# Optimization experiments

Measured on AMD Instinct MI355X. Metric: run time of the kernel, lower is better.

Reference implementation:

```python
import jax, jax.numpy as jnp
import numpy as np

D_MODEL = 2048
N_HEADS = 16
HEAD_DIM = D_MODEL // N_HEADS  # 128
SCALE_BASE = 512


def rotate_half(x):
    x1, x2 = jnp.split(x, 2, axis=-1)
    return jnp.concatenate((-x2, x1), axis=-1)


def rotary_xpos(seq_len, dim, dtype=jnp.float32):
    inv_freq = 1.0 / (10000.0 ** (jnp.arange(0, dim, 2, dtype=jnp.float32) / dim))
    t = jnp.arange(seq_len, dtype=jnp.float32)
    freqs = jnp.einsum('i,j->ij', t, inv_freq)
    freqs = jnp.concatenate((freqs, freqs), axis=-1)  # [S, dim]
    scale_base = (jnp.arange(0, dim, 2, dtype=jnp.float32) + 0.4 * dim) / (1.4 * dim)
    power = (t - seq_len // 2) / SCALE_BASE
    scale = scale_base[None, :] ** power[:, None]  # [S, dim/2]
    scale = jnp.concatenate((scale, scale), axis=-1)  # [S, dim]
    return freqs.astype(dtype), scale.astype(dtype)


def apply_rotary(t, pos, scale):
    return t * jnp.cos(pos) * scale + rotate_half(t) * jnp.sin(pos) * scale


def setup_inputs() -> dict:
    key = jax.random.key(0)
    ks = jax.random.split(key, 5)
    B, S = 2, 2048
    hidden_states = jax.random.normal(ks[0], (B, S, D_MODEL), dtype=jnp.float32)
    # Linear weights stored as [out, in] like torch; we use x @ W.T
    w_q = jax.random.normal(ks[1], (N_HEADS * HEAD_DIM, D_MODEL), dtype=jnp.float32) * 0.02
    w_kv = jax.random.normal(ks[2], (2 * HEAD_DIM, D_MODEL), dtype=jnp.float32) * 0.02
    w_proj = jax.random.normal(ks[3], (D_MODEL, N_HEADS * HEAD_DIM), dtype=jnp.float32) * 0.02
    b_proj = jax.random.normal(ks[4], (D_MODEL,), dtype=jnp.float32) * 0.02
    return {"hidden_states": hidden_states, "w_q": w_q, "w_kv": w_kv,
            "w_proj": w_proj, "b_proj": b_proj}


def reference(hidden_states, w_q, w_kv, w_proj, b_proj):
    B, S, _ = hidden_states.shape
    q = hidden_states @ w_q.T                      # [B,S,H*D]
    kv = hidden_states @ w_kv.T                    # [B,S,2*D]
    k, v = jnp.split(kv, 2, axis=-1)               # [B,S,D] each
    q = q.reshape(B, S, N_HEADS, HEAD_DIM).transpose(0, 2, 1, 3)  # [B,H,S,D]

    scale_w = HEAD_DIM ** (-0.5)
    q = q * scale_w
    k = k * scale_w

    pos, xscale = rotary_xpos(S, HEAD_DIM, q.dtype)
    q = apply_rotary(q, pos, xscale)               # broadcast [S,D] over [B,H,S,D]
    k = apply_rotary(k, pos, 1.0 / xscale)         # [B,S,D]

    attn = jnp.einsum('bnih,bjh->bnij', q, k)      # [B,H,S,S]
    causal = jnp.triu(jnp.ones((S, S), dtype=bool), 1)
    attn = jnp.where(causal, -jnp.finfo(attn.dtype).max, attn)
    attn = jax.nn.softmax(attn, axis=-1)

    out = jnp.einsum('bnij,bjd->bind', attn, v)    # [B,S,H,D]
    out = out.reshape(B, S, N_HEADS * HEAD_DIM)
    out = out @ w_proj.T + b_proj
    return out
```

## Files before the change

### kernel.cpp

```cpp
#include <hip/hip_runtime.h>
#include <math.h>

typedef __bf16 bf16;
typedef __bf16 bf16x8 __attribute__((ext_vector_type(8)));
typedef float f32x4 __attribute__((ext_vector_type(4)));

#define MFMA16(a, b, c) __builtin_amdgcn_mfma_f32_16x16x32_bf16((a), (b), (c), 0, 0, 0)

__device__ __forceinline__ float clampf(float v, float lo, float hi) {
  return fminf(fmaxf(v, lo), hi);
}

__device__ __forceinline__ void async_copy16(const void* g, void* l) {
  __builtin_amdgcn_global_load_lds(
      (__attribute__((address_space(1))) void*)g,
      (__attribute__((address_space(3))) void*)l,
      16, 0, 0);
}


__global__ void convert_bf16(const float* __restrict__ hs,
                             const float* __restrict__ wq,
                             const float* __restrict__ wkv,
                             const float* __restrict__ wproj,
                             bf16* __restrict__ hs_bf,
                             bf16* __restrict__ wqkv_bf,
                             bf16* __restrict__ wproj_bf) {
  const long long v = (long long)blockIdx.x * blockDim.x + threadIdx.x;
  const float* src;
  bf16* dst;
  long long off;
  if (v < 1048576) { src = hs; dst = hs_bf; off = v; }
  else if (v < 1572864) { src = wq; dst = wqkv_bf; off = v - 1048576; }
  else if (v < 1638400) { src = wkv; dst = wqkv_bf + 4194304; off = v - 1572864; }
  else { src = wproj; dst = wproj_bf; off = v - 1638400; }
  const f32x4* p = (const f32x4*)(src + off * 8);
  f32x4 f0 = p[0], f1 = p[1];
  bf16x8 r;
#pragma unroll
  for (int i = 0; i < 4; ++i) { r[i] = (bf16)f0[i]; r[i + 4] = (bf16)f1[i]; }
  *(bf16x8*)(dst + off * 8) = r;
}

__global__ __launch_bounds__(256, 2)
void gemm_qkv(const bf16* __restrict__ A, const bf16* __restrict__ Bw,
              bf16* __restrict__ Cq, bf16* __restrict__ Ckv) {
  const int K = 2048;
  __shared__ bf16 As[128 * 32];
  __shared__ bf16 Bs[128 * 32];
  const int tid = threadIdx.x;
  const int wave = tid >> 6, lane = tid & 63;
  const int quad = lane >> 4, l15 = lane & 15;
  const int r4 = lane >> 2, c4 = lane & 3;
  const int wm = wave >> 1, wn = wave & 1;
  const int orig = blockIdx.x + 18 * blockIdx.y;
  const int wgid = (orig & 7) * 72 + (orig >> 3);
  const int bx = wgid % 18;
  const int bm = (wgid / 18) * 128;
  const bf16* Bp = Bw + (size_t)bx * 128 * K;

  const f32x4 vzero = {0.f, 0.f, 0.f, 0.f};
  f32x4 acc[4][4];
#pragma unroll
  for (int i = 0; i < 4; ++i)
#pragma unroll
    for (int j = 0; j < 4; ++j) acc[i][j] = vzero;

  for (int kt = 0; kt < K; kt += 32) {
    __syncthreads();
#pragma unroll
    for (int q = 0; q < 2; ++q) {
      const int chunk = wave * 2 + q;
      const int row = chunk * 16 + r4;
      async_copy16(A + (size_t)(bm + row) * K + kt + c4 * 8, (char*)As + chunk * 1024);
      async_copy16(Bp + (size_t)row * K + kt + c4 * 8, (char*)Bs + chunk * 1024);
    }
    __syncthreads();
    bf16x8 af[4], bfr[4];
#pragma unroll
    for (int i = 0; i < 4; ++i)
      af[i] = *(const bf16x8*)((const char*)As + (wm * 64 + i * 16 + l15) * 64 + quad * 16);
#pragma unroll
    for (int i = 0; i < 4; ++i)
      bfr[i] = *(const bf16x8*)((const char*)Bs + (wn * 64 + i * 16 + l15) * 64 + quad * 16);
#pragma unroll
    for (int mi = 0; mi < 4; ++mi)
#pragma unroll
      for (int ni = 0; ni < 4; ++ni)
        acc[mi][ni] = MFMA16(af[mi], bfr[ni], acc[mi][ni]);
  }

  bf16* Cp;
  int ldc, cn;
  if (bx < 16) { Cp = Cq; ldc = 2048; cn = bx * 128; }
  else { Cp = Ckv; ldc = 256; cn = (bx - 16) * 128; }
#pragma unroll
  for (int mi = 0; mi < 4; ++mi)
#pragma unroll
    for (int ni = 0; ni < 4; ++ni) {
      const int col = cn + wn * 64 + ni * 16 + l15;
#pragma unroll
      for (int r = 0; r < 4; ++r) {
        const int row = bm + wm * 64 + mi * 16 + quad * 4 + r;
        Cp[(size_t)row * ldc + col] = (bf16)clampf(acc[mi][ni][r], -1000.f, 1000.f);
      }
    }
}

__global__ __launch_bounds__(256, 2)
void gemm_proj(const bf16* __restrict__ A, const bf16* __restrict__ Bw,
               const float* __restrict__ bias, float* __restrict__ C) {
  const int K = 2048;
  __shared__ bf16 As[128 * 32];
  __shared__ bf16 Bs[128 * 32];
  const int tid = threadIdx.x;
  const int wave = tid >> 6, lane = tid & 63;
  const int quad = lane >> 4, l15 = lane & 15;
  const int r4 = lane >> 2, c4 = lane & 3;
  const int wm = wave >> 1, wn = wave & 1;
  const int orig = blockIdx.x + 16 * blockIdx.y;
  const int wgid = (orig & 7) * 64 + (orig >> 3);
  const int bn = (wgid % 16) * 128;
  const int bm = (wgid / 16) * 128;
  const bf16* Bp = Bw + (size_t)bn * K;

  const f32x4 vzero = {0.f, 0.f, 0.f, 0.f};
  f32x4 acc[4][4];
#pragma unroll
  for (int i = 0; i < 4; ++i)
#pragma unroll
    for (int j = 0; j < 4; ++j) acc[i][j] = vzero;

  for (int kt = 0; kt < K; kt += 32) {
    __syncthreads();
#pragma unroll
    for (int q = 0; q < 2; ++q) {
      const int chunk = wave * 2 + q;
      const int row = chunk * 16 + r4;
      async_copy16(A + (size_t)(bm + row) * K + kt + c4 * 8, (char*)As + chunk * 1024);
      async_copy16(Bp + (size_t)row * K + kt + c4 * 8, (char*)Bs + chunk * 1024);
    }
    __syncthreads();
    bf16x8 af[4], bfr[4];
#pragma unroll
    for (int i = 0; i < 4; ++i)
      af[i] = *(const bf16x8*)((const char*)As + (wm * 64 + i * 16 + l15) * 64 + quad * 16);
#pragma unroll
    for (int i = 0; i < 4; ++i)
      bfr[i] = *(const bf16x8*)((const char*)Bs + (wn * 64 + i * 16 + l15) * 64 + quad * 16);
#pragma unroll
    for (int mi = 0; mi < 4; ++mi)
#pragma unroll
      for (int ni = 0; ni < 4; ++ni)
        acc[mi][ni] = MFMA16(af[mi], bfr[ni], acc[mi][ni]);
  }

#pragma unroll
  for (int mi = 0; mi < 4; ++mi)
#pragma unroll
    for (int ni = 0; ni < 4; ++ni) {
      const int col = bn + wn * 64 + ni * 16 + l15;
      const float bv = bias[col];
#pragma unroll
      for (int r = 0; r < 4; ++r) {
        const int row = bm + wm * 64 + mi * 16 + quad * 4 + r;
        C[(size_t)row * 2048 + col] = clampf(acc[mi][ni][r] + bv, -1000.f, 1000.f);
      }
    }
}

__global__ void rotary_kv(bf16* __restrict__ Ckv, bf16* __restrict__ VT) {
  const int row = blockIdx.x;
  const int b = row >> 11, s = row & 2047;
  const int t = threadIdx.x;

  if (t < 64) {
    const float power = (float)(s - 1024) * (1.0f / 512.0f);
    const float scale_w = 0.08838834764831845f;
    const float k_if = 0.2076205059304679f;
    const int j = t;
    const float pos = (float)s * exp2f(-k_if * (float)j);
    const float c = cosf(pos), sn = sinf(pos);
    const float sb = ((float)(2 * j) + 51.2f) * (1.0f / 179.2f);
    const float xs = exp2f(power * log2f(sb));
    const float f = scale_w / xs;
    const size_t kvb = (size_t)row * 256;
    const float k1 = (float)Ckv[kvb + j];
    const float k2 = (float)Ckv[kvb + j + 64];
    Ckv[kvb + j]      = (bf16)((k1 * c - k2 * sn) * f);
    Ckv[kvb + j + 64] = (bf16)((k2 * c + k1 * sn) * f);
  } else {
    const int d = (t - 64) * 2;
    const size_t kvb = (size_t)row * 256 + 128;
    VT[((size_t)b * 128 + d) * 2048 + s]     = Ckv[kvb + d];
    VT[((size_t)b * 128 + d + 1) * 2048 + s] = Ckv[kvb + d + 1];
  }
}

__global__ __launch_bounds__(512, 1)
void flash_attn(const bf16* __restrict__ Qp, const bf16* __restrict__ Kkv,
                const bf16* __restrict__ VT, bf16* __restrict__ O) {
  __shared__ bf16 Ks[2][4 * 64 * 32];
  __shared__ bf16 Vs[2][2 * 128 * 32];
  __shared__ bf16 Ps[8][1024];

  const int tid = threadIdx.x;
  const int wave = tid >> 6, lane = tid & 63;
  const int quad = lane >> 4, l15 = lane & 15;
  const int r4 = lane >> 2, c4 = lane & 3;
  const int bh = blockIdx.x, b = bh >> 4, h = bh & 15;
  const int y = blockIdx.y;
  const int nkvA = 2 * y + 2;
  const int wrow = wave * 16;

  const int ssw = (r4 >> 1) & 3;
  const int rsw = ((l15 >> 1) & 3) * 16;

  const bf16* Kb = Kkv + (size_t)b * 2048 * 256;
  const bf16* Vb = VT + (size_t)b * 128 * 2048;

  bf16x8 vones;
  {
    const bf16 ov = (bf16)((l15 == 0) ? 1.0f : 0.0f);
#pragma unroll
    for (int i = 0; i < 8; ++i) vones[i] = ov;
  }

  const f32x4 vzero = {0.f, 0.f, 0.f, 0.f};
  bf16x8 qa[4];
  f32x4 oacc[8];
  f32x4 lacc;

  auto load_q = [&](int q0) {
    const int s = q0 + wrow + l15;
#pragma unroll
    for (int ks = 0; ks < 4; ++ks)
      qa[ks] = *(const bf16x8*)(Qp + ((size_t)(b * 2048 + s)) * 2048 +
                                h * 128 + ks * 32 + quad * 8);
    const float power = (float)(s - 1024) * (1.0f / 512.0f);
    const float scale_w = 0.08838834764831845f;
    const float k_if = 0.2076205059304679f;
#pragma unroll
    for (int ks = 0; ks < 2; ++ks)
#pragma unroll
      for (int u = 0; u < 8; ++u) {
        const int j = ks * 32 + quad * 8 + u;
        const float pos = (float)s * exp2f(-k_if * (float)j);
        const float c = __cosf(pos), sn = __sinf(pos);
        const float sb = ((float)(2 * j) + 51.2f) * (1.0f / 179.2f);
        const float xs = exp2f(power * __log2f(sb));
        const float f = xs * scale_w;
        const float q1 = (float)qa[ks][u], q2 = (float)qa[ks + 2][u];
        qa[ks][u]     = (bf16)((q1 * c - q2 * sn) * f);
        qa[ks + 2][u] = (bf16)((q2 * c + q1 * sn) * f);
      }
  };
  auto reset_acc = [&]() {
    lacc = vzero;
#pragma unroll
    for (int n8 = 0; n8 < 8; ++n8) oacc[n8] = vzero;
  };

  auto stage = [&](int kv0, int buf) {
#pragma unroll
    for (int t = 0; t < 2; ++t) {
      const int ii = wave * 2 + t;
      const int p = ii >> 2, ch = ii & 3;
      async_copy16(Kb + (size_t)(kv0 + ch * 16 + r4) * 256 + p * 32 + (c4 ^ ssw) * 8,
                   (char*)Ks[buf] + ii * 1024);
    }
#pragma unroll
    for (int t = 0; t < 2; ++t) {
      const int ii = wave * 2 + t;
      const int pc = ii >> 3, ch = ii & 7;
      async_copy16(Vb + (size_t)(ch * 16 + r4) * 2048 + kv0 + pc * 32 + (c4 ^ ssw) * 8,
                   (char*)Vs[buf] + ii * 1024);
    }
  };

  auto epilogue = [&](int q0) {
#pragma unroll
    for (int r = 0; r < 4; ++r) {
      const float l = __shfl(lacc[r], lane & 48);
      const float inv = 1.0f / l;
      const int s = q0 + wrow + quad * 4 + r;
#pragma unroll
      for (int n8 = 0; n8 < 8; ++n8) {
        const int d = n8 * 16 + l15;
        O[((size_t)(b * 2048 + s)) * 2048 + h * 128 + d] = (bf16)(oacc[n8][r] * inv);
      }
    }
  };

  int q0 = y * 128;
  load_q(q0);
  reset_acc();
  stage(0, 0);

  for (int jt = 0; jt < 34; ++jt) {
    const int kv0 = (jt < nkvA ? jt : jt - nkvA) * 64;
    const int buf = jt & 1;
    __syncthreads();
    if (jt + 1 < 34) {
      const int njt = jt + 1;
      stage((njt < nkvA ? njt : njt - nkvA) * 64, buf ^ 1);
    }

    if (kv0 <= q0 + wrow + 15) {
      f32x4 sacc[4];
#pragma unroll
      for (int ns = 0; ns < 4; ++ns) sacc[ns] = vzero;
      __builtin_amdgcn_s_setprio(1);
#pragma unroll
      for (int ks = 0; ks < 4; ++ks) {
        bf16x8 kb[4];
#pragma unroll
        for (int ns = 0; ns < 4; ++ns)
          kb[ns] = *(const bf16x8*)((const char*)Ks[buf] + ks * 4096 +
                                    (ns * 16 + l15) * 64 + (quad * 16 ^ rsw));
#pragma unroll
        for (int ns = 0; ns < 4; ++ns)
          sacc[ns] = MFMA16(qa[ks], kb[ns], sacc[ns]);
      }
      __builtin_amdgcn_s_setprio(0);
      if (kv0 + 63 > q0 + wrow) {
#pragma unroll
        for (int ns = 0; ns < 4; ++ns)
#pragma unroll
          for (int r = 0; r < 4; ++r) {
            const int qg = q0 + wrow + quad * 4 + r;
            const int kg = kv0 + ns * 16 + l15;
            sacc[ns][r] = (kg > qg) ? 0.0f : __expf(sacc[ns][r]);
          }
      } else {
#pragma unroll
        for (int ns = 0; ns < 4; ++ns)
#pragma unroll
          for (int r = 0; r < 4; ++r)
            sacc[ns][r] = __expf(sacc[ns][r]);
      }
#pragma unroll
      for (int ns = 0; ns < 4; ++ns)
#pragma unroll
        for (int r = 0; r < 4; ++r) {
          const int row = quad * 4 + r;
          const int slot = (ns & 1) * 2 + (l15 >> 3);
          *(bf16*)((char*)Ps[wave] + (ns >> 1) * 1024 + row * 64 +
                   ((slot ^ ((row >> 1) & 3)) * 16) + (l15 & 7) * 2) = (bf16)sacc[ns][r];
        }
#pragma unroll
      for (int ks2 = 0; ks2 < 2; ++ks2) {
        bf16x8 pa, vb[8];
        pa = *(const bf16x8*)((const char*)Ps[wave] + ks2 * 1024 + l15 * 64 +
                              (quad * 16 ^ rsw));
#pragma unroll
        for (int n8 = 0; n8 < 8; ++n8)
          vb[n8] = *(const bf16x8*)((const char*)Vs[buf] + ks2 * 8192 +
                                    (n8 * 16 + l15) * 64 + (quad * 16 ^ rsw));
        __builtin_amdgcn_s_setprio(1);
#pragma unroll
        for (int n8 = 0; n8 < 8; ++n8)
          oacc[n8] = MFMA16(pa, vb[n8], oacc[n8]);
        lacc = MFMA16(pa, vones, lacc);
        __builtin_amdgcn_s_setprio(0);
      }
    }

    if (jt == nkvA - 1) {
      epilogue(q0);
      reset_acc();
      q0 = (15 - y) * 128;
      load_q(q0);
    }
  }
  epilogue(q0);
}

extern "C" void kernel_launch(void* const* d_in, const int* in_sizes, int n_in,
                              void* d_out, int out_size, void* d_ws, size_t ws_size,
                              hipStream_t stream) {
  const float* hs     = (const float*)d_in[0];
  const float* w_q    = (const float*)d_in[1];
  const float* w_kv   = (const float*)d_in[2];
  const float* w_proj = (const float*)d_in[3];
  const float* b_proj = (const float*)d_in[4];
  float* out = (float*)d_out;
  bf16* Qbuf  = (bf16*)d_out;
  bf16* hs_bf = (bf16*)((char*)d_out + 16777216);

  char* ws = (char*)d_ws;
  bf16* Ckv      = (bf16*)(ws);
  bf16* VT       = (bf16*)(ws + 2097152);
  bf16* AO       = (bf16*)(ws + 3145728);
  bf16* wqkv_bf  = (bf16*)(ws + 19922944);
  bf16* wproj_bf = (bf16*)(ws + 29360128);

  convert_bf16<<<dim3(8448), dim3(256), 0, stream>>>(hs, w_q, w_kv, w_proj,
                                                     hs_bf, wqkv_bf, wproj_bf);
  gemm_qkv<<<dim3(18, 32), dim3(256), 0, stream>>>(hs_bf, wqkv_bf, Qbuf, Ckv);
  rotary_kv<<<dim3(4096), dim3(128), 0, stream>>>(Ckv, VT);
  flash_attn<<<dim3(32, 8), dim3(512), 0, stream>>>(Qbuf, Ckv, VT, AO);
  gemm_proj<<<dim3(16, 32), dim3(256), 0, stream>>>(AO, wproj_bf, b_proj, out);
}
```

Before: 271.8 us.

## Double-buffer LDS tiles and XOR-swizzle layout in QKV and projection GEMMs

Both bf16 GEMM kernels now keep two LDS buffers per operand. They issue the async global-to-LDS copy of the next K-tile before computing on the current one, which drops one barrier per iteration. The 16-byte chunks in LDS are XOR-swizzled by row, and the fragment reads are unswizzled to match, to reduce bank conflicts. LDS use doubles, which may limit occupancy. The compiler may also insert conservative waits that limit the intended overlap.

```diff
diff --git a/kernel.cpp b/kernel.cpp
--- a/kernel.cpp
+++ b/kernel.cpp
@@ -46,8 +46,8 @@
 void gemm_qkv(const bf16* __restrict__ A, const bf16* __restrict__ Bw,
               bf16* __restrict__ Cq, bf16* __restrict__ Ckv) {
   const int K = 2048;
-  __shared__ bf16 As[128 * 32];
-  __shared__ bf16 Bs[128 * 32];
+  __shared__ bf16 As[2][128 * 32];
+  __shared__ bf16 Bs[2][128 * 32];
   const int tid = threadIdx.x;
   const int wave = tid >> 6, lane = tid & 63;
   const int quad = lane >> 4, l15 = lane & 15;
@@ -59,6 +59,9 @@
   const int bm = (wgid / 18) * 128;
   const bf16* Bp = Bw + (size_t)bx * 128 * K;
 
+  const int ssw = (r4 >> 1) & 3;
+  const int rsw = ((l15 >> 1) & 3) * 16;
+
   const f32x4 vzero = {0.f, 0.f, 0.f, 0.f};
   f32x4 acc[4][4];
 #pragma unroll
@@ -66,23 +69,31 @@
 #pragma unroll
     for (int j = 0; j < 4; ++j) acc[i][j] = vzero;
 
-  for (int kt = 0; kt < K; kt += 32) {
+  auto stage = [&](int kt, int buf) {
+#pragma unroll
+    for (int t = 0; t < 2; ++t) {
+      const int ii = wave * 2 + t;
+      const int row = ii * 16 + r4;
+      async_copy16(A + (size_t)(bm + row) * K + kt + (c4 ^ ssw) * 8,
+                   (char*)As[buf] + ii * 1024);
+      async_copy16(Bp + (size_t)row * K + kt + (c4 ^ ssw) * 8,
+                   (char*)Bs[buf] + ii * 1024);
+    }
+  };
+
+  stage(0, 0);
+  for (int it = 0; it < 64; ++it) {
+    const int buf = it & 1;
     __syncthreads();
-#pragma unroll
-    for (int q = 0; q < 2; ++q) {
-      const int chunk = wave * 2 + q;
-      const int row = chunk * 16 + r4;
-      async_copy16(A + (size_t)(bm + row) * K + kt + c4 * 8, (char*)As + chunk * 1024);
-      async_copy16(Bp + (size_t)row * K + kt + c4 * 8, (char*)Bs + chunk * 1024);
-    }
-    __syncthreads();
+    if (it + 1 < 64) stage((it + 1) * 32, buf ^ 1);
     bf16x8 af[4], bfr[4];
 #pragma unroll
-    for (int i = 0; i < 4; ++i)
-      af[i] = *(const bf16x8*)((const char*)As + (wm * 64 + i * 16 + l15) * 64 + quad * 16);
-#pragma unroll
-    for (int i = 0; i < 4; ++i)
-      bfr[i] = *(const bf16x8*)((const char*)Bs + (wn * 64 + i * 16 + l15) * 64 + quad * 16);
+    for (int i = 0; i < 4; ++i) {
+      af[i] = *(const bf16x8*)((const char*)As[buf] +
+                               (wm * 64 + i * 16 + l15) * 64 + (quad * 16 ^ rsw));
+      bfr[i] = *(const bf16x8*)((const char*)Bs[buf] +
+                                (wn * 64 + i * 16 + l15) * 64 + (quad * 16 ^ rsw));
+    }
 #pragma unroll
     for (int mi = 0; mi < 4; ++mi)
 #pragma unroll
@@ -111,8 +122,8 @@
 void gemm_proj(const bf16* __restrict__ A, const bf16* __restrict__ Bw,
                const float* __restrict__ bias, float* __restrict__ C) {
   const int K = 2048;
-  __shared__ bf16 As[128 * 32];
-  __shared__ bf16 Bs[128 * 32];
+  __shared__ bf16 As[2][128 * 32];
+  __shared__ bf16 Bs[2][128 * 32];
   const int tid = threadIdx.x;
   const int wave = tid >> 6, lane = tid & 63;
   const int quad = lane >> 4, l15 = lane & 15;
@@ -124,6 +135,9 @@
   const int bm = (wgid / 16) * 128;
   const bf16* Bp = Bw + (size_t)bn * K;
 
+  const int ssw = (r4 >> 1) & 3;
+  const int rsw = ((l15 >> 1) & 3) * 16;
+
   const f32x4 vzero = {0.f, 0.f, 0.f, 0.f};
   f32x4 acc[4][4];
 #pragma unroll
@@ -131,23 +145,31 @@
 #pragma unroll
     for (int j = 0; j < 4; ++j) acc[i][j] = vzero;
 
-  for (int kt = 0; kt < K; kt += 32) {
+  auto stage = [&](int kt, int buf) {
+#pragma unroll
+    for (int t = 0; t < 2; ++t) {
+      const int ii = wave * 2 + t;
+      const int row = ii * 16 + r4;
+      async_copy16(A + (size_t)(bm + row) * K + kt + (c4 ^ ssw) * 8,
+                   (char*)As[buf] + ii * 1024);
+      async_copy16(Bp + (size_t)row * K + kt + (c4 ^ ssw) * 8,
+                   (char*)Bs[buf] + ii * 1024);
+    }
+  };
+
+  stage(0, 0);
+  for (int it = 0; it < 64; ++it) {
+    const int buf = it & 1;
     __syncthreads();
-#pragma unroll
-    for (int q = 0; q < 2; ++q) {
-      const int chunk = wave * 2 + q;
-      const int row = chunk * 16 + r4;
-      async_copy16(A + (size_t)(bm + row) * K + kt + c4 * 8, (char*)As + chunk * 1024);
-      async_copy16(Bp + (size_t)row * K + kt + c4 * 8, (char*)Bs + chunk * 1024);
-    }
-    __syncthreads();
+    if (it + 1 < 64) stage((it + 1) * 32, buf ^ 1);
     bf16x8 af[4], bfr[4];
 #pragma unroll
-    for (int i = 0; i < 4; ++i)
-      af[i] = *(const bf16x8*)((const char*)As + (wm * 64 + i * 16 + l15) * 64 + quad * 16);
-#pragma unroll
-    for (int i = 0; i < 4; ++i)
-      bfr[i] = *(const bf16x8*)((const char*)Bs + (wn * 64 + i * 16 + l15) * 64 + quad * 16);
+    for (int i = 0; i < 4; ++i) {
+      af[i] = *(const bf16x8*)((const char*)As[buf] +
+                               (wm * 64 + i * 16 + l15) * 64 + (quad * 16 ^ rsw));
+      bfr[i] = *(const bf16x8*)((const char*)Bs[buf] +
+                                (wn * 64 + i * 16 + l15) * 64 + (quad * 16 ^ rsw));
+    }
 #pragma unroll
     for (int mi = 0; mi < 4; ++mi)
 #pragma unroll
```

Result: slower. 279.2 us (+2.7%).
